# Optimization experiments

Hardware: AMD Instinct MI355X
Metric: run time of the kernel (lower is better)

Reference implementation:

```python
import math
import jax, jax.numpy as jnp
import numpy as np

DEGREE = 5
LN_EPS = 1e-5


def hermite_psi(C, r):
    # x_d = tanh(linspace(-1,1,C)) * (sqrt(2r+1)+1), shape [C]
    x_d = jnp.tanh(jnp.linspace(-1.0, 1.0, C)) * (math.sqrt(2 * r + 1) + 1.0)
    g = jnp.exp(-x_d ** 2 / 2.0)
    rows = [math.pi ** (-0.25) * g]
    if r > 0:
        rows.append(math.sqrt(2.0) * math.pi ** (-0.25) * x_d * g)
    for k in range(2, r + 1):
        rows.append(math.sqrt(2.0 / k) * x_d * rows[-1] - math.sqrt((k - 1) / k) * rows[-2])
    return jnp.stack(rows)  # [r+1, C]


def setup_inputs() -> dict:
    key = jax.random.key(0)
    k1, k2 = jax.random.split(key)
    B, C, H, W = 16, 512, 64, 64
    O = 512
    x = jax.random.normal(k1, (B, C, H, W), dtype=jnp.float32)
    ln_w = jnp.ones((C,), dtype=jnp.float32)
    ln_b = jnp.zeros((C,), dtype=jnp.float32)
    fc_w = jax.random.normal(k2, (O, C), dtype=jnp.float32) * (1.0 / math.sqrt(C))
    fc_b = jnp.zeros((O,), dtype=jnp.float32)
    return {"x": x, "ln_w": ln_w, "ln_b": ln_b, "fc_w": fc_w, "fc_b": fc_b}


def reference(x, ln_w, ln_b, fc_w, fc_b):
    B, C, H, W = x.shape
    O = fc_w.shape[0]
    # [B, HW, C]
    q = x.reshape(B, C, H * W).transpose(0, 2, 1)
    # LayerNorm over channels (biased variance, eps=1e-5)
    mu = q.mean(axis=-1, keepdims=True)
    var = ((q - mu) ** 2).mean(axis=-1, keepdims=True)
    q = (q - mu) / jnp.sqrt(var + LN_EPS) * ln_w + ln_b
    # Constant Hermite basis [r+1, C]
    psi = hermite_psi(C, DEGREE).astype(x.dtype)
    # Tiny cross-attention: scores [B, HW, r+1]
    scores = jnp.einsum('bnc,rc->bnr', q, psi) / math.sqrt(C)
    attn = jax.nn.softmax(scores, axis=-1)
    y = jnp.einsum('bnr,rc->bnc', attn, psi)  # [B, HW, C]
    # 1x1 conv == pointwise GEMM over channels
    out = jnp.einsum('bnc,oc->bon', y, fc_w) + fc_b[None, :, None]
    return out.reshape(B, O, H, W)
```

## Files before the change

kernel.cpp:

```cpp
#include <hip/hip_runtime.h>
#include <math.h>

#define C 512
#define NPIX 4096
#define BATCH 16
#define O 512
#define R 6
#define LN_EPS 1e-5f

typedef float vf2 __attribute__((ext_vector_type(2)));


__device__ __forceinline__ void hermite_rows(int c, float rows[R]) {
    float t = -1.0f + 2.0f * (float)c / 511.0f;
    float xd = tanhf(t) * 4.31662479035539984911f;
    float g = expf(-0.5f * xd * xd);
    const float pi_m14 = 0.75112554446494248286f;
    rows[0] = pi_m14 * g;
    rows[1] = 1.41421356237309504880f * pi_m14 * xd * g;
    #pragma unroll
    for (int k = 2; k <= 5; ++k)
        rows[k] = sqrtf(2.0f / k) * xd * rows[k - 1] - sqrtf((k - 1.0f) / k) * rows[k - 2];
}

__global__ __launch_bounds__(64) void setup_all(const float* __restrict__ lnw,
                                                const float* __restrict__ lnb,
                                                const float* __restrict__ fcw,
                                                const float* __restrict__ fcb,
                                                float* __restrict__ ws) {
    const int o = blockIdx.x;
    const int l = threadIdx.x;
    if (o < O) {
        float acc[R] = {0.f, 0.f, 0.f, 0.f, 0.f, 0.f};
        #pragma unroll
        for (int k = 0; k < 8; ++k) {
            int c = l + (k << 6);
            float rows[R];
            hermite_rows(c, rows);
            float w = fcw[o * C + c];
            #pragma unroll
            for (int r = 0; r < R; ++r) acc[r] += rows[r] * w;
        }
        #pragma unroll
        for (int r = 0; r < R; ++r)
            #pragma unroll
            for (int m = 32; m >= 1; m >>= 1) acc[r] += __shfl_xor(acc[r], m, 64);
        if (l == 0) {
            float bias = fcb[o];
            float* M = ws + 4112 + o * 8;
            #pragma unroll
            for (int r = 0; r < R; ++r) M[r] = acc[r] + bias;
        }
    } else {
        float sw[R] = {0.f, 0.f, 0.f, 0.f, 0.f, 0.f};
        float sb[R] = {0.f, 0.f, 0.f, 0.f, 0.f, 0.f};
        #pragma unroll
        for (int k = 0; k < 8; ++k) {
            int c = l + (k << 6);
            float rows[R];
            hermite_rows(c, rows);
            float w = lnw[c], bb = lnb[c];
            float* dst = ws + c * 8;
            #pragma unroll
            for (int r = 0; r < R; ++r) {
                float rw = rows[r] * w;
                dst[r] = rw;
                sw[r] += rw;
                sb[r] += rows[r] * bb;
            }
        }
        #pragma unroll
        for (int r = 0; r < R; ++r) {
            #pragma unroll
            for (int m = 32; m >= 1; m >>= 1) {
                sw[r] += __shfl_xor(sw[r], m, 64);
                sb[r] += __shfl_xor(sb[r], m, 64);
            }
        }
        if (l == 0) {
            #pragma unroll
            for (int r = 0; r < R; ++r) { ws[4096 + r] = sw[r]; ws[4104 + r] = sb[r]; }
        }
    }
}

__global__ __launch_bounds__(1024, 8) void fused_kernel(const float* __restrict__ x,
                                                        const float* __restrict__ ws,
                                                        float* __restrict__ out) {
    __shared__ float part[16][8][128];
    __shared__ float attn_s[R][128];
    const int tid = threadIdx.x;
    const int wv = tid >> 6;
    const int l = tid & 63;
    const int b = blockIdx.x >> 5;
    const int pxg = blockIdx.x & 31;
    const int n0 = pxg << 7;
    const int p2 = l << 1;
    const int wuni = __builtin_amdgcn_readfirstlane(wv);

    const float* xb = x + (((size_t)(b * C + (wuni << 5))) << 12) + n0 + p2;
    const float* wbase = ws + ((size_t)(wuni << 5) << 3);

    float sx = 0.f, sy = 0.f, ssx = 0.f, ssy = 0.f;
    float a0x = 0.f, a0y = 0.f, a1x = 0.f, a1y = 0.f, a2x = 0.f, a2y = 0.f;
    float a3x = 0.f, a3y = 0.f, a4x = 0.f, a4y = 0.f, a5x = 0.f, a5y = 0.f;
    #pragma unroll
    for (int i = 0; i < 32; ++i) {
        vf2 xv = *(const vf2*)(xb + ((size_t)i << 12));
        const float* wr = wbase + (i << 3);
        float w0 = wr[0], w1 = wr[1], w2 = wr[2];
        float w3 = wr[3], w4 = wr[4], w5 = wr[5];
        sx += xv.x;          sy += xv.y;
        ssx += xv.x * xv.x;  ssy += xv.y * xv.y;
        a0x += xv.x * w0;    a0y += xv.y * w0;
        a1x += xv.x * w1;    a1y += xv.y * w1;
        a2x += xv.x * w2;    a2y += xv.y * w2;
        a3x += xv.x * w3;    a3y += xv.y * w3;
        a4x += xv.x * w4;    a4y += xv.y * w4;
        a5x += xv.x * w5;    a5y += xv.y * w5;
    }
    {
        vf2 t;
        t.x = sx;  t.y = sy;  *(vf2*)&part[wv][0][p2] = t;
        t.x = ssx; t.y = ssy; *(vf2*)&part[wv][1][p2] = t;
        t.x = a0x; t.y = a0y; *(vf2*)&part[wv][2][p2] = t;
        t.x = a1x; t.y = a1y; *(vf2*)&part[wv][3][p2] = t;
        t.x = a2x; t.y = a2y; *(vf2*)&part[wv][4][p2] = t;
        t.x = a3x; t.y = a3y; *(vf2*)&part[wv][5][p2] = t;
        t.x = a4x; t.y = a4y; *(vf2*)&part[wv][6][p2] = t;
        t.x = a5x; t.y = a5y; *(vf2*)&part[wv][7][p2] = t;
    }
    __syncthreads();

    if (tid < 128) {
        float v[8];
        #pragma unroll
        for (int st = 0; st < 8; ++st) {
            float acc = 0.f;
            #pragma unroll
            for (int w = 0; w < 16; ++w) acc += part[w][st][tid];
            v[st] = acc;
        }
        float mu = v[0] * (1.0f / 512.0f);
        float var = v[1] * (1.0f / 512.0f) - mu * mu;
        float rsig = rsqrtf(var + LN_EPS);
        const float invsq = 0.04419417382415922f;
        float sc[R], mx = -1e30f;
        #pragma unroll
        for (int r = 0; r < R; ++r) {
            float swp = ws[4096 + r], sbp = ws[4104 + r];
            sc[r] = ((v[2 + r] - mu * swp) * rsig + sbp) * invsq;
            mx = fmaxf(mx, sc[r]);
        }
        float es = 0.f, at[R];
        #pragma unroll
        for (int r = 0; r < R; ++r) { at[r] = expf(sc[r] - mx); es += at[r]; }
        float inv = 1.0f / es;
        #pragma unroll
        for (int r = 0; r < R; ++r) attn_s[r][tid] = at[r] * inv;
    }
    __syncthreads();

    float arx[R], ary[R];
    #pragma unroll
    for (int r = 0; r < R; ++r) {
        vf2 a = *(const vf2*)&attn_s[r][p2];
        arx[r] = a.x; ary[r] = a.y;
    }
    const float* Ms = ws + 4112 + ((size_t)(wuni << 5) << 3);
    float* ob = out + (((size_t)(b * O + (wuni << 5))) << 12) + n0 + p2;
    #pragma unroll
    for (int j = 0; j < 32; ++j) {
        const float* mo = Ms + (j << 3);
        float m0 = mo[0], m1 = mo[1], m2 = mo[2];
        float m3 = mo[3], m4 = mo[4], m5 = mo[5];
        vf2 res;
        res.x = arx[0] * m0 + arx[1] * m1 + arx[2] * m2
              + arx[3] * m3 + arx[4] * m4 + arx[5] * m5;
        res.y = ary[0] * m0 + ary[1] * m1 + ary[2] * m2
              + ary[3] * m3 + ary[4] * m4 + ary[5] * m5;
        __builtin_nontemporal_store(res, (vf2*)(ob + ((size_t)j << 12)));
    }
}

extern "C" void kernel_launch(void* const* d_in, const int* in_sizes, int n_in,
                              void* d_out, int out_size, void* d_ws, size_t ws_size,
                              hipStream_t stream) {
    const float* x    = (const float*)d_in[0];
    const float* ln_w = (const float*)d_in[1];
    const float* ln_b = (const float*)d_in[2];
    const float* fc_w = (const float*)d_in[3];
    const float* fc_b = (const float*)d_in[4];
    float* out = (float*)d_out;
    float* ws = (float*)d_ws;

    setup_all<<<O + 1, 64, 0, stream>>>(ln_w, ln_b, fc_w, fc_b, ws);
    fused_kernel<<<BATCH * 32, 1024, 0, stream>>>(x, ws, out);
}
```

Before: 252.0 us.

## Process two pixel tiles per block, overlapping stores of first with loads of second

```diff
diff --git a/kernel.cpp b/kernel.cpp
--- a/kernel.cpp
+++ b/kernel.cpp
@@ -84,7 +84,7 @@
     }
 }
 
-__global__ __launch_bounds__(1024, 8) void fused_kernel(const float* __restrict__ x,
+__global__ __launch_bounds__(1024, 4) void fused_kernel(const float* __restrict__ x,
                                                         const float* __restrict__ ws,
                                                         float* __restrict__ out) {
     __shared__ float part[16][8][128];
@@ -92,34 +92,40 @@
     const int tid = threadIdx.x;
     const int wv = tid >> 6;
     const int l = tid & 63;
-    const int b = blockIdx.x >> 5;
-    const int pxg = blockIdx.x & 31;
-    const int n0 = pxg << 7;
+    const int b = blockIdx.x >> 4;
+    const int sg = blockIdx.x & 15;
+    const int n0 = sg << 8;
     const int p2 = l << 1;
     const int wuni = __builtin_amdgcn_readfirstlane(wv);
 
-    const float* xb = x + (((size_t)(b * C + (wuni << 5))) << 12) + n0 + p2;
+    const float* xw = x + (((size_t)(b * C + (wuni << 5))) << 12);
+    float* ow = out + (((size_t)(b * O + (wuni << 5))) << 12);
     const float* wbase = ws + ((size_t)(wuni << 5) << 3);
-
-    float sx = 0.f, sy = 0.f, ssx = 0.f, ssy = 0.f;
-    float a0x = 0.f, a0y = 0.f, a1x = 0.f, a1y = 0.f, a2x = 0.f, a2y = 0.f;
-    float a3x = 0.f, a3y = 0.f, a4x = 0.f, a4y = 0.f, a5x = 0.f, a5y = 0.f;
-    #pragma unroll
-    for (int i = 0; i < 32; ++i) {
-        vf2 xv = *(const vf2*)(xb + ((size_t)i << 12));
-        const float* wr = wbase + (i << 3);
-        float w0 = wr[0], w1 = wr[1], w2 = wr[2];
-        float w3 = wr[3], w4 = wr[4], w5 = wr[5];
-        sx += xv.x;          sy += xv.y;
-        ssx += xv.x * xv.x;  ssy += xv.y * xv.y;
-        a0x += xv.x * w0;    a0y += xv.y * w0;
-        a1x += xv.x * w1;    a1y += xv.y * w1;
-        a2x += xv.x * w2;    a2y += xv.y * w2;
-        a3x += xv.x * w3;    a3y += xv.y * w3;
-        a4x += xv.x * w4;    a4y += xv.y * w4;
-        a5x += xv.x * w5;    a5y += xv.y * w5;
-    }
+    const float* Ms = ws + 4112 + ((size_t)(wuni << 5) << 3);
+
+    float sx, sy, ssx, ssy;
+    float a0x, a0y, a1x, a1y, a2x, a2y, a3x, a3y, a4x, a4y, a5x, a5y;
+
     {
+        const float* xb = xw + n0 + p2;
+        sx = sy = ssx = ssy = 0.f;
+        a0x = a0y = a1x = a1y = a2x = a2y = 0.f;
+        a3x = a3y = a4x = a4y = a5x = a5y = 0.f;
+        #pragma unroll
+        for (int i = 0; i < 32; ++i) {
+            vf2 xv = *(const vf2*)(xb + ((size_t)i << 12));
+            const float* wr = wbase + (i << 3);
+            float w0 = wr[0], w1 = wr[1], w2 = wr[2];
+            float w3 = wr[3], w4 = wr[4], w5 = wr[5];
+            sx += xv.x;          sy += xv.y;
+            ssx += xv.x * xv.x;  ssy += xv.y * xv.y;
+            a0x += xv.x * w0;    a0y += xv.y * w0;
+            a1x += xv.x * w1;    a1y += xv.y * w1;
+            a2x += xv.x * w2;    a2y += xv.y * w2;
+            a3x += xv.x * w3;    a3y += xv.y * w3;
+            a4x += xv.x * w4;    a4y += xv.y * w4;
+            a5x += xv.x * w5;    a5y += xv.y * w5;
+        }
         vf2 t;
         t.x = sx;  t.y = sy;  *(vf2*)&part[wv][0][p2] = t;
         t.x = ssx; t.y = ssy; *(vf2*)&part[wv][1][p2] = t;
@@ -167,19 +173,98 @@
         vf2 a = *(const vf2*)&attn_s[r][p2];
         arx[r] = a.x; ary[r] = a.y;
     }
-    const float* Ms = ws + 4112 + ((size_t)(wuni << 5) << 3);
-    float* ob = out + (((size_t)(b * O + (wuni << 5))) << 12) + n0 + p2;
+
+    {
+        const float* xb = xw + n0 + 128 + p2;
+        float* ob = ow + n0 + p2;
+        sx = sy = ssx = ssy = 0.f;
+        a0x = a0y = a1x = a1y = a2x = a2y = 0.f;
+        a3x = a3y = a4x = a4y = a5x = a5y = 0.f;
+        #pragma unroll
+        for (int i = 0; i < 32; ++i) {
+            vf2 xv = *(const vf2*)(xb + ((size_t)i << 12));
+            const float* mo = Ms + (i << 3);
+            float m0 = mo[0], m1 = mo[1], m2 = mo[2];
+            float m3 = mo[3], m4 = mo[4], m5 = mo[5];
+            vf2 res;
+            res.x = arx[0] * m0 + arx[1] * m1 + arx[2] * m2
+                  + arx[3] * m3 + arx[4] * m4 + arx[5] * m5;
+            res.y = ary[0] * m0 + ary[1] * m1 + ary[2] * m2
+                  + ary[3] * m3 + ary[4] * m4 + ary[5] * m5;
+            __builtin_nontemporal_store(res, (vf2*)(ob + ((size_t)i << 12)));
+            const float* wr = wbase + (i << 3);
+            float w0 = wr[0], w1 = wr[1], w2 = wr[2];
+            float w3 = wr[3], w4 = wr[4], w5 = wr[5];
+            sx += xv.x;          sy += xv.y;
+            ssx += xv.x * xv.x;  ssy += xv.y * xv.y;
+            a0x += xv.x * w0;    a0y += xv.y * w0;
+            a1x += xv.x * w1;    a1y += xv.y * w1;
+            a2x += xv.x * w2;    a2y += xv.y * w2;
+            a3x += xv.x * w3;    a3y += xv.y * w3;
+            a4x += xv.x * w4;    a4y += xv.y * w4;
+            a5x += xv.x * w5;    a5y += xv.y * w5;
+        }
+        vf2 t;
+        t.x = sx;  t.y = sy;  *(vf2*)&part[wv][0][p2] = t;
+        t.x = ssx; t.y = ssy; *(vf2*)&part[wv][1][p2] = t;
+        t.x = a0x; t.y = a0y; *(vf2*)&part[wv][2][p2] = t;
+        t.x = a1x; t.y = a1y; *(vf2*)&part[wv][3][p2] = t;
+        t.x = a2x; t.y = a2y; *(vf2*)&part[wv][4][p2] = t;
+        t.x = a3x; t.y = a3y; *(vf2*)&part[wv][5][p2] = t;
+        t.x = a4x; t.y = a4y; *(vf2*)&part[wv][6][p2] = t;
+        t.x = a5x; t.y = a5y; *(vf2*)&part[wv][7][p2] = t;
+    }
+    __syncthreads();
+
+    if (tid < 128) {
+        float v[8];
+        #pragma unroll
+        for (int st = 0; st < 8; ++st) {
+            float acc = 0.f;
+            #pragma unroll
+            for (int w = 0; w < 16; ++w) acc += part[w][st][tid];
+            v[st] = acc;
+        }
+        float mu = v[0] * (1.0f / 512.0f);
+        float var = v[1] * (1.0f / 512.0f) - mu * mu;
+        float rsig = rsqrtf(var + LN_EPS);
+        const float invsq = 0.04419417382415922f;
+        float sc[R], mx = -1e30f;
+        #pragma unroll
+        for (int r = 0; r < R; ++r) {
+            float swp = ws[4096 + r], sbp = ws[4104 + r];
+            sc[r] = ((v[2 + r] - mu * swp) * rsig + sbp) * invsq;
+            mx = fmaxf(mx, sc[r]);
+        }
+        float es = 0.f, at[R];
+        #pragma unroll
+        for (int r = 0; r < R; ++r) { at[r] = expf(sc[r] - mx); es += at[r]; }
+        float inv = 1.0f / es;
+        #pragma unroll
+        for (int r = 0; r < R; ++r) attn_s[r][tid] = at[r] * inv;
+    }
+    __syncthreads();
+
     #pragma unroll
-    for (int j = 0; j < 32; ++j) {
-        const float* mo = Ms + (j << 3);
-        float m0 = mo[0], m1 = mo[1], m2 = mo[2];
-        float m3 = mo[3], m4 = mo[4], m5 = mo[5];
-        vf2 res;
-        res.x = arx[0] * m0 + arx[1] * m1 + arx[2] * m2
-              + arx[3] * m3 + arx[4] * m4 + arx[5] * m5;
-        res.y = ary[0] * m0 + ary[1] * m1 + ary[2] * m2
-              + ary[3] * m3 + ary[4] * m4 + ary[5] * m5;
-        __builtin_nontemporal_store(res, (vf2*)(ob + ((size_t)j << 12)));
+    for (int r = 0; r < R; ++r) {
+        vf2 a = *(const vf2*)&attn_s[r][p2];
+        arx[r] = a.x; ary[r] = a.y;
+    }
+
+    {
+        float* ob = ow + n0 + 128 + p2;
+        #pragma unroll
+        for (int j = 0; j < 32; ++j) {
+            const float* mo = Ms + (j << 3);
+            float m0 = mo[0], m1 = mo[1], m2 = mo[2];
+            float m3 = mo[3], m4 = mo[4], m5 = mo[5];
+            vf2 res;
+            res.x = arx[0] * m0 + arx[1] * m1 + arx[2] * m2
+                  + arx[3] * m3 + arx[4] * m4 + arx[5] * m5;
+            res.y = ary[0] * m0 + ary[1] * m1 + ary[2] * m2
+                  + ary[3] * m3 + ary[4] * m4 + ary[5] * m5;
+            __builtin_nontemporal_store(res, (vf2*)(ob + ((size_t)j << 12)));
+        }
     }
 }
 
@@ -195,5 +280,5 @@
     float* ws = (float*)d_ws;
 
     setup_all<<<O + 1, 64, 0, stream>>>(ln_w, ln_b, fc_w, fc_b, ws);
-    fused_kernel<<<BATCH * 32, 1024, 0, stream>>>(x, ws, out);
-}
+    fused_kernel<<<BATCH * 16, 1024, 0, stream>>>(x, ws, out);
+}
```

Result: faster. 247.1 us (-2.0%).
